# Performance work log

Hardware: AMD Instinct MI355X
Metric: run time of the kernel (lower is better)

The kernel has to match this reference:

```python
import jax, jax.numpy as jnp
import numpy as np

N_A, N_B = 50000, 10000
E = 300000
IN_F, HID, BEL_OUT, INC_OUT = 256, 256, 128, 128


def _gconv(x_src, W, b, src, dst, n_src, n_dst):
    """DGL GraphConv with norm='both': D_in^{-1/2} A D_out^{-1/2} X W + b, degs clamped to >=1."""
    ones = jnp.ones(src.shape[0], x_src.dtype)
    deg_out = jnp.maximum(jax.ops.segment_sum(ones, src, num_segments=n_src), 1.0)
    deg_in = jnp.maximum(jax.ops.segment_sum(ones, dst, num_segments=n_dst), 1.0)
    h = (x_src * jax.lax.rsqrt(deg_out)[:, None]) @ W        # [n_src, out]
    agg = jax.ops.segment_sum(h[src], dst, num_segments=n_dst)  # scatter-add messages
    return agg * jax.lax.rsqrt(deg_in)[:, None] + b


def setup_inputs() -> dict:
    key = jax.random.key(0)
    ks = jax.random.split(key, 12)
    s = 1.0 / np.sqrt(IN_F)
    sh = 1.0 / np.sqrt(HID)
    return {
        "x_a": jax.random.normal(ks[0], (N_A, IN_F), jnp.float32),
        "x_b": jax.random.normal(ks[1], (N_B, IN_F), jnp.float32),
        "W1_bel": jax.random.normal(ks[2], (IN_F, HID), jnp.float32) * s,
        "b1_bel": jnp.zeros((HID,), jnp.float32),
        "W1_inc": jax.random.normal(ks[3], (IN_F, HID), jnp.float32) * s,
        "b1_inc": jnp.zeros((HID,), jnp.float32),
        "W2_bel": jax.random.normal(ks[4], (HID, BEL_OUT), jnp.float32) * sh,
        "b2_bel": jnp.zeros((BEL_OUT,), jnp.float32),
        "W2_inc": jax.random.normal(ks[5], (HID, INC_OUT), jnp.float32) * sh,
        "b2_inc": jnp.zeros((INC_OUT,), jnp.float32),
        "bel_src": jax.random.randint(ks[6], (E,), 0, N_A, jnp.int32),
        "bel_dst": jax.random.randint(ks[7], (E,), 0, N_B, jnp.int32),
        "inc_src": jax.random.randint(ks[8], (E,), 0, N_B, jnp.int32),
        "inc_dst": jax.random.randint(ks[9], (E,), 0, N_A, jnp.int32),
    }


def reference(x_a, x_b, W1_bel, b1_bel, W1_inc, b1_inc, W2_bel, b2_bel,
              W2_inc, b2_inc, bel_src, bel_dst, inc_src, inc_dst):
    n_a, n_b = x_a.shape[0], x_b.shape[0]
    # layer 1 (HeteroGraphConv, mean over a single relation per dst type = identity)
    h_b = _gconv(x_a, W1_bel, b1_bel, bel_src, bel_dst, n_a, n_b)  # 'belongs_to': A->B
    h_a = _gconv(x_b, W1_inc, b1_inc, inc_src, inc_dst, n_b, n_a)  # 'including' : B->A
    h_a = jax.nn.relu(h_a)
    h_b = jax.nn.relu(h_b)
    # layer 2
    out_b = _gconv(h_a, W2_bel, b2_bel, bel_src, bel_dst, n_a, n_b)  # [N_B, bel_out]
    out_a = _gconv(h_b, W2_inc, b2_inc, inc_src, inc_dst, n_b, n_a)  # [N_A, inc_out]
    return out_a, out_b
```

## Files before the change

### kernel.cpp

```cpp
#include <hip/hip_runtime.h>


#define NA 50000
#define NB 10000
#define NE 300000
#define CVTB 400

typedef unsigned short u16;
typedef unsigned int u32;
typedef __attribute__((ext_vector_type(8))) short short8;
typedef __attribute__((ext_vector_type(4))) float f32x4;
typedef __attribute__((ext_vector_type(2))) float f32x2;
typedef __attribute__((ext_vector_type(4))) unsigned short u16x4;
typedef __attribute__((ext_vector_type(2))) unsigned short u16x2;

__device__ __forceinline__ float bf2f(u16 h){
  union { u32 u; float f; } x; x.u = ((u32)h) << 16; return x.f;
}
__device__ __forceinline__ u16 f2bf(float f){
  union { float f; u32 u; } x; x.f = f;
  u32 r = (x.u + 0x7FFFu + ((x.u >> 16) & 1u)) >> 16;
  return (u16)r;
}

__global__ __launch_bounds__(256) void setup0_kernel(
    int* __restrict__ z, int nz,
    const float* __restrict__ W1b, const float* __restrict__ W1i,
    const float* __restrict__ W2b, const float* __restrict__ W2i,
    u16* __restrict__ pwh, u16* __restrict__ pwl){
  int g = blockIdx.x * blockDim.x + threadIdx.x;
  int s = gridDim.x * blockDim.x;
  for (int i = g; i < nz; i += s) z[i] = 0;
  const int total = 65536 + 65536 + 32768 + 32768;
  for (int t = g; t < total; t += s){
    const float* W; int N; int tt;
    if (t < 65536)       { W = W1b; N = 256; tt = t; }
    else if (t < 131072) { W = W1i; N = 256; tt = t - 65536; }
    else if (t < 163840) { W = W2b; N = 128; tt = t - 131072; }
    else                 { W = W2i; N = 128; tt = t - 163840; }
    int j = tt & 7, lane = (tt >> 3) & 63, tile = tt >> 9;
    int nT = N >> 4;
    int nt = tile % nT, kt = tile / nT;
    int k = kt * 32 + ((lane >> 4) << 3) + j;
    int n = nt * 16 + (lane & 15);
    float v = W[k * N + n];
    u16 hi = f2bf(v);
    pwh[t] = hi;
    pwl[t] = f2bf(v - bf2f(hi));
  }
}

__global__ void hist_kernel(const int* __restrict__ bs, const int* __restrict__ bd,
                            const int* __restrict__ isc, const int* __restrict__ idt,
                            int* __restrict__ c_bs, int* __restrict__ c_bd,
                            int* __restrict__ c_is, int* __restrict__ c_id){
  int g = blockIdx.x * blockDim.x + threadIdx.x;
  int s = gridDim.x * blockDim.x;
  for (int e = g; e < NE; e += s){
    atomicAdd(&c_bs[bs[e]], 1);
    atomicAdd(&c_bd[bd[e]], 1);
    atomicAdd(&c_is[isc[e]], 1);
    atomicAdd(&c_id[idt[e]], 1);
  }
}

__global__ __launch_bounds__(1024) void scan_scales_kernel(
    const int* __restrict__ c_bs, const int* __restrict__ c_bd,
    const int* __restrict__ c_is, const int* __restrict__ c_id,
    int* __restrict__ off_bel, int* __restrict__ off_inc,
    float* __restrict__ s_ob, float* __restrict__ s_ib,
    float* __restrict__ s_oi, float* __restrict__ s_ii){
  if (blockIdx.x >= 2){
    int g = (blockIdx.x - 2) * blockDim.x + threadIdx.x;
    int s = (gridDim.x - 2) * blockDim.x;
    for (int i = g; i < NA; i += s){
      int a = c_bs[i]; s_ob[i] = rsqrtf((float)(a > 1 ? a : 1));
      int b = c_id[i]; s_ii[i] = rsqrtf((float)(b > 1 ? b : 1));
      if (i < NB){
        int c = c_bd[i]; s_ib[i] = rsqrtf((float)(c > 1 ? c : 1));
        int d = c_is[i]; s_oi[i] = rsqrtf((float)(d > 1 ? d : 1));
      }
    }
    return;
  }
  const int* cnt; int* off; int n;
  if (blockIdx.x == 0){ cnt = c_bd; off = off_bel; n = NB; }
  else                { cnt = c_id; off = off_inc; n = NA; }
  __shared__ int wsum[16];
  __shared__ int carry, chunkTot;
  int tid = threadIdx.x, lane = tid & 63, wid = tid >> 6;
  if (tid == 0) carry = 0;
  __syncthreads();
  for (int base = 0; base < n; base += 4096){
    int i0 = base + tid * 4;
    int v[4];
#pragma unroll
    for (int r = 0; r < 4; ++r){ int idx = i0 + r; v[r] = (idx < n) ? cnt[idx] : 0; }
    int s = v[0] + v[1] + v[2] + v[3];
    int x = s;
#pragma unroll
    for (int d = 1; d < 64; d <<= 1){ int t = __shfl_up(x, d, 64); if (lane >= d) x += t; }
    if (lane == 63) wsum[wid] = x;
    __syncthreads();
    if (wid == 0){
      int ws = (lane < 16) ? wsum[lane] : 0;
#pragma unroll
      for (int d = 1; d < 16; d <<= 1){ int t = __shfl_up(ws, d, 64); if (lane >= d) ws += t; }
      if (lane < 16) wsum[lane] = ws;
      if (lane == 15) chunkTot = ws;
    }
    __syncthreads();
    int waveBase = (wid == 0) ? 0 : wsum[wid - 1];
    int run = carry + waveBase + (x - s);
#pragma unroll
    for (int r = 0; r < 4; ++r){ int idx = i0 + r; if (idx < n) off[idx] = run; run += v[r]; }
    __syncthreads();
    if (tid == 0) carry += chunkTot;
    __syncthreads();
  }
  if (tid == 0) off[n] = carry;
}

__global__ __launch_bounds__(256) void cvt_fill_kernel(
    const float* __restrict__ xa, const float* __restrict__ s_ob,
    u16* __restrict__ xa16,
    const int* __restrict__ bs, const int* __restrict__ bd,
    const int* __restrict__ isc, const int* __restrict__ idt,
    const int* __restrict__ off_bel, const int* __restrict__ off_inc,
    int* __restrict__ cur_bel, int* __restrict__ cur_inc,
    int* __restrict__ csr_bel, int* __restrict__ csr_inc){
  if (blockIdx.x < CVTB){
    int g = (blockIdx.x * blockDim.x + threadIdx.x) * 4;
    int s = CVTB * blockDim.x * 4;
    for (int i = g; i < NA * 256; i += s){
      float4 v = *(const float4*)(xa + i);
      float sc = s_ob[i >> 8];
      u16x4 o;
      o.x = f2bf(v.x * sc); o.y = f2bf(v.y * sc);
      o.z = f2bf(v.z * sc); o.w = f2bf(v.w * sc);
      __builtin_nontemporal_store(o, (u16x4*)(xa16 + i));
    }
  } else {
    int g = (blockIdx.x - CVTB) * blockDim.x + threadIdx.x;
    int s = (gridDim.x - CVTB) * blockDim.x;
    for (int e = g; e < NE; e += s){
      int d0 = bd[e];
      int p0 = off_bel[d0] + atomicAdd(&cur_bel[d0], 1);
      csr_bel[p0] = bs[e];
      int d1 = idt[e];
      int p1 = off_inc[d1] + atomicAdd(&cur_inc[d1], 1);
      csr_inc[p1] = isc[e];
    }
  }
}

__global__ __launch_bounds__(256) void agg_bel_kernel(
    const u16* __restrict__ X, const int* __restrict__ off,
    const int* __restrict__ csr, float* __restrict__ Pf, int nDst){
  int wave = blockIdx.x * 4 + (threadIdx.x >> 6);
  int lane = threadIdx.x & 63;
  if (wave >= nDst) return;
  int b0 = off[wave], b1 = off[wave + 1];
  int deg = b1 - b0;
  int part = lane >> 5;
  int cl = lane & 31;
  int c = cl * 8;
  float acc[8];
#pragma unroll
  for (int q = 0; q < 8; ++q) acc[q] = 0.f;
  int idx = 0;
  if (lane < deg) idx = csr[b0 + lane];
  int lim = deg < 64 ? deg : 64;
  for (int u = 0; u < lim; u += 8){
    const u16* addr[4]; float w[4];
#pragma unroll
    for (int k = 0; k < 4; ++k){
      int e = u + k * 2 + part;
      int t = e < lim ? e : 0;
      int s0 = __shfl(idx, t, 64);
      w[k] = e < lim ? 1.f : 0.f;
      addr[k] = X + (size_t)s0 * 256 + c;
    }
    short8 v[4];
#pragma unroll
    for (int k = 0; k < 4; ++k) v[k] = *(const short8*)addr[k];
#pragma unroll
    for (int k = 0; k < 4; ++k)
#pragma unroll
      for (int q = 0; q < 8; ++q) acc[q] += bf2f((u16)v[k][q]) * w[k];
  }
  for (int j = b0 + 64 + part; j < b1; j += 2){
    int s0 = csr[j];
    short8 v0 = *(const short8*)(X + (size_t)s0 * 256 + c);
#pragma unroll
    for (int q = 0; q < 8; ++q) acc[q] += bf2f((u16)v0[q]);
  }
#pragma unroll
  for (int q = 0; q < 8; ++q) acc[q] += __shfl_xor(acc[q], 32, 64);
  if (part == 0){
    f32x4 f0 = {acc[0], acc[1], acc[2], acc[3]};
    f32x4 f1 = {acc[4], acc[5], acc[6], acc[7]};
    __builtin_nontemporal_store(f0, (f32x4*)(Pf + (size_t)wave * 256 + c));
    __builtin_nontemporal_store(f1, (f32x4*)(Pf + (size_t)wave * 256 + c + 4));
  }
}

__global__ __launch_bounds__(256) void agg_inc2_kernel(
    const u16* __restrict__ G12, const int* __restrict__ off,
    const int* __restrict__ csr,
    const float* __restrict__ s_ii, const float* __restrict__ s_ob,
    const float* __restrict__ b1i, const float* __restrict__ b2i,
    u16* __restrict__ Ha, float* __restrict__ outa){
  int wave = blockIdx.x * 4 + (threadIdx.x >> 6);
  int lane = threadIdx.x & 63;
  if (wave >= NA) return;
  int b0 = off[wave], b1 = off[wave + 1];
  int deg = b1 - b0;
  int c1 = lane * 4;
  int c2 = lane * 2;
  float acc[6];
#pragma unroll
  for (int q = 0; q < 6; ++q) acc[q] = 0.f;
  int idx = 0;
  if (lane < deg) idx = csr[b0 + lane];
  int lim = deg < 64 ? deg : 64;
  for (int u = 0; u < lim; u += 4){
    ushort4 va[4]; ushort2 vb[4]; float w[4];
#pragma unroll
    for (int k = 0; k < 4; ++k){
      int e = u + k;
      int t = e < lim ? e : 0;
      int se = __shfl(idx, t, 64);
      w[k] = e < lim ? 1.f : 0.f;
      const u16* r = G12 + (size_t)se * 384;
      va[k] = *(const ushort4*)(r + c1);
      vb[k] = *(const ushort2*)(r + 256 + c2);
    }
#pragma unroll
    for (int k = 0; k < 4; ++k){
      acc[0] += bf2f(va[k].x) * w[k];
      acc[1] += bf2f(va[k].y) * w[k];
      acc[2] += bf2f(va[k].z) * w[k];
      acc[3] += bf2f(va[k].w) * w[k];
      acc[4] += bf2f(vb[k].x) * w[k];
      acc[5] += bf2f(vb[k].y) * w[k];
    }
  }
  for (int j = b0 + 64; j < b1; ++j){
    int se = csr[j];
    const u16* r = G12 + (size_t)se * 384;
    ushort4 va = *(const ushort4*)(r + c1);
    ushort2 vb = *(const ushort2*)(r + 256 + c2);
    acc[0] += bf2f(va.x); acc[1] += bf2f(va.y);
    acc[2] += bf2f(va.z); acc[3] += bf2f(va.w);
    acc[4] += bf2f(vb.x); acc[5] += bf2f(vb.y);
  }
  float sii = s_ii[wave], sob = s_ob[wave];
  float4 bb1 = *(const float4*)(b1i + c1);
  f32x2 bb2 = *(const f32x2*)(b2i + c2);
  u16x4 o1;
  o1.x = f2bf(fmaxf(acc[0] * sii + bb1.x, 0.f) * sob);
  o1.y = f2bf(fmaxf(acc[1] * sii + bb1.y, 0.f) * sob);
  o1.z = f2bf(fmaxf(acc[2] * sii + bb1.z, 0.f) * sob);
  o1.w = f2bf(fmaxf(acc[3] * sii + bb1.w, 0.f) * sob);
  __builtin_nontemporal_store(o1, (u16x4*)(Ha + (size_t)wave * 256 + c1));
  f32x2 o2 = {acc[4] * sii + bb2.x, acc[5] * sii + bb2.y};
  __builtin_nontemporal_store(o2, (f32x2*)(outa + (size_t)wave * 128 + c2));
}

__global__ __launch_bounds__(256) void gemm_kernel(
    const float* __restrict__ A,
    const u16* __restrict__ PWH, const u16* __restrict__ PWL,
    const float* __restrict__ bias, const float* __restrict__ rs,
    float* __restrict__ Cf, u16* __restrict__ C16,
    int M, int nT, int wpsShift, int doRelu, int ldC, int colOff){
  int wave = blockIdx.x * 4 + (threadIdx.x >> 6);
  int lane = threadIdx.x & 63;
  int strips = M >> 4;
  int strip = wave >> wpsShift;
  if (strip >= strips) return;
  int slice = wave & ((1 << wpsShift) - 1);
  int ntPer = nT >> wpsShift;
  int ntStart = slice * ntPer;
  int r16 = lane & 15, quad = lane >> 4;
  int m0 = strip << 4;
  const float* aBase = A + (size_t)(m0 + r16) * 256 + quad * 8;
  short8 ah[8], al[8];
#pragma unroll
  for (int kt = 0; kt < 8; ++kt){
    float4 p0 = *(const float4*)(aBase + kt * 32);
    float4 p1 = *(const float4*)(aBase + kt * 32 + 4);
    float v[8] = {p0.x, p0.y, p0.z, p0.w, p1.x, p1.y, p1.z, p1.w};
    short8 h, l;
#pragma unroll
    for (int j = 0; j < 8; ++j){
      u16 hb = f2bf(v[j]);
      h[j] = (short)hb;
      l[j] = (short)f2bf(v[j] - bf2f(hb));
    }
    ah[kt] = h; al[kt] = l;
  }
  float rscale[4];
#pragma unroll
  for (int r = 0; r < 4; ++r) rscale[r] = rs ? rs[m0 + quad * 4 + r] : 1.f;
  for (int nt = ntStart; nt < ntStart + ntPer; ++nt){
    f32x4 acc = {0.f, 0.f, 0.f, 0.f};
    const u16* bh = PWH + ((size_t)nt * 64 + lane) * 8;
    const u16* bl = PWL + ((size_t)nt * 64 + lane) * 8;
#pragma unroll
    for (int kt = 0; kt < 8; ++kt){
      short8 wh = *(const short8*)(bh + (size_t)kt * nT * 512);
      short8 wl = *(const short8*)(bl + (size_t)kt * nT * 512);
      acc = __builtin_amdgcn_mfma_f32_16x16x32_bf16(ah[kt], wh, acc, 0, 0, 0);
      acc = __builtin_amdgcn_mfma_f32_16x16x32_bf16(al[kt], wh, acc, 0, 0, 0);
      acc = __builtin_amdgcn_mfma_f32_16x16x32_bf16(ah[kt], wl, acc, 0, 0, 0);
    }
    int col = nt * 16 + r16;
    float bv = bias ? bias[col] : 0.f;
#pragma unroll
    for (int r = 0; r < 4; ++r){
      float v = acc[r] * rscale[r] + bv;
      if (doRelu) v = fmaxf(v, 0.f);
      size_t o = (size_t)(m0 + quad * 4 + r) * ldC + colOff + col;
      if (C16) __builtin_nontemporal_store(f2bf(v), C16 + o);
      else     __builtin_nontemporal_store(v, Cf + o);
    }
  }
}

extern "C" void kernel_launch(void* const* d_in, const int* in_sizes, int n_in,
                              void* d_out, int out_size, void* d_ws, size_t ws_size,
                              hipStream_t stream){
  const float* x_a = (const float*)d_in[0];
  const float* x_b = (const float*)d_in[1];
  const float* W1b = (const float*)d_in[2];
  const float* b1b = (const float*)d_in[3];
  const float* W1i = (const float*)d_in[4];
  const float* b1i = (const float*)d_in[5];
  const float* W2b = (const float*)d_in[6];
  const float* b2b = (const float*)d_in[7];
  const float* W2i = (const float*)d_in[8];
  const float* b2i = (const float*)d_in[9];
  const int* bs  = (const int*)d_in[10];
  const int* bd  = (const int*)d_in[11];
  const int* isc = (const int*)d_in[12];
  const int* idt = (const int*)d_in[13];

  char* w = (char*)d_ws;
  size_t o = 0;
  auto take = [&](size_t bytes) -> void* {
    void* p = w + o; o = (o + bytes + 255) & ~(size_t)255; return p;
  };
  int* zint = (int*)take(180000 * sizeof(int));
  int* c_bs = zint, *c_bd = zint + 50000, *c_is = zint + 60000, *c_id = zint + 70000;
  int* cur_bel = zint + 120000, *cur_inc = zint + 130000;
  int* off_bel = (int*)take((NB + 1) * sizeof(int));
  int* off_inc = (int*)take((NA + 1) * sizeof(int));
  int* csr_bel = (int*)take(NE * sizeof(int));
  int* csr_inc = (int*)take(NE * sizeof(int));
  float* s_ob = (float*)take(NA * sizeof(float));
  float* s_ib = (float*)take(NB * sizeof(float));
  float* s_oi = (float*)take(NB * sizeof(float));
  float* s_ii = (float*)take(NA * sizeof(float));
  u16* pwh = (u16*)take(196608 * sizeof(u16));
  u16* pwl = (u16*)take(196608 * sizeof(u16));
  u16* pwh1b = pwh, *pwh1i = pwh + 65536, *pwh2b = pwh + 131072, *pwh2i = pwh + 163840;
  u16* pwl1b = pwl, *pwl1i = pwl + 65536, *pwl2b = pwl + 131072, *pwl2i = pwl + 163840;
  u16* xa16 = (u16*)take((size_t)NA * 256 * sizeof(u16));
  u16* G12  = (u16*)take((size_t)NB * 384 * sizeof(u16));
  u16* H_a  = (u16*)take((size_t)NA * 256 * sizeof(u16));
  float* P_b = (float*)take((size_t)NB * 256 * sizeof(float));
  float* H_b = (float*)take((size_t)NB * 256 * sizeof(float));

  float* out_a = (float*)d_out;
  float* out_b = (float*)d_out + (size_t)NA * 128;

  setup0_kernel<<<512, 256, 0, stream>>>(zint, 180000, W1b, W1i, W2b, W2i, pwh, pwl);
  hist_kernel<<<1172, 256, 0, stream>>>(bs, bd, isc, idt, c_bs, c_bd, c_is, c_id);
  scan_scales_kernel<<<52, 1024, 0, stream>>>(c_bs, c_bd, c_is, c_id,
                                              off_bel, off_inc,
                                              s_ob, s_ib, s_oi, s_ii);
  cvt_fill_kernel<<<CVTB + 1172, 256, 0, stream>>>(x_a, s_ob, xa16,
                                                   bs, bd, isc, idt,
                                                   off_bel, off_inc,
                                                   cur_bel, cur_inc,
                                                   csr_bel, csr_inc);

  gemm_kernel<<<625, 256, 0, stream>>>(x_b, pwh1i, pwl1i, nullptr, s_oi,
                                       nullptr, G12, NB, 16, 2, 0, 384, 0);
  agg_bel_kernel<<<2500, 256, 0, stream>>>(xa16, off_bel, csr_bel, P_b, NB);
  gemm_kernel<<<625, 256, 0, stream>>>(P_b, pwh1b, pwl1b, b1b, s_ib,
                                       H_b, nullptr, NB, 16, 2, 1, 256, 0);
  gemm_kernel<<<625, 256, 0, stream>>>(H_b, pwh2i, pwl2i, nullptr, s_oi,
                                       nullptr, G12, NB, 8, 2, 0, 384, 256);
  agg_inc2_kernel<<<12500, 256, 0, stream>>>(G12, off_inc, csr_inc,
                                             s_ii, s_ob, b1i, b2i, H_a, out_a);
  agg_bel_kernel<<<2500, 256, 0, stream>>>(H_a, off_bel, csr_bel, P_b, NB);
  gemm_kernel<<<625, 256, 0, stream>>>(P_b, pwh2b, pwl2b, b2b, s_ib,
                                       out_b, nullptr, NB, 8, 2, 0, 128, 0);
}
```

Measured before the change: 432.0 us.

## Record atomic ranks in histogram, overlap x_a conversion, apply out-degree scale in aggregation

The histogram kernel now stores each edge's atomic rank within its destination bucket, so CSR fill becomes an atomic-free scatter using offset plus rank. The x_a to bf16 conversion moves into the histogram launch, because it no longer needs the out-degree scale and can run alongside the histogram. The scale is instead applied per source edge inside the first bel aggregation, which adds a gather of s_ob per edge. The change also adds two rank arrays the size of the edge list, costing extra memory traffic.

Result: faster. 409.4 us (-5.2%).

```diff
diff --git a/kernel.cpp b/kernel.cpp
--- a/kernel.cpp
+++ b/kernel.cpp
@@ -4,6 +4,7 @@
 #define NA 50000
 #define NB 10000
 #define NE 300000
+#define HB 1172
 #define CVTB 400
 
 typedef unsigned short u16;
@@ -12,7 +13,6 @@
 typedef __attribute__((ext_vector_type(4))) float f32x4;
 typedef __attribute__((ext_vector_type(2))) float f32x2;
 typedef __attribute__((ext_vector_type(4))) unsigned short u16x4;
-typedef __attribute__((ext_vector_type(2))) unsigned short u16x2;
 
 __device__ __forceinline__ float bf2f(u16 h){
   union { u32 u; float f; } x; x.u = ((u32)h) << 16; return x.f;
@@ -50,17 +50,31 @@
   }
 }
 
-__global__ void hist_kernel(const int* __restrict__ bs, const int* __restrict__ bd,
-                            const int* __restrict__ isc, const int* __restrict__ idt,
-                            int* __restrict__ c_bs, int* __restrict__ c_bd,
-                            int* __restrict__ c_is, int* __restrict__ c_id){
-  int g = blockIdx.x * blockDim.x + threadIdx.x;
-  int s = gridDim.x * blockDim.x;
-  for (int e = g; e < NE; e += s){
-    atomicAdd(&c_bs[bs[e]], 1);
-    atomicAdd(&c_bd[bd[e]], 1);
-    atomicAdd(&c_is[isc[e]], 1);
-    atomicAdd(&c_id[idt[e]], 1);
+__global__ __launch_bounds__(256) void histcvt_kernel(
+    const int* __restrict__ bs, const int* __restrict__ bd,
+    const int* __restrict__ isc, const int* __restrict__ idt,
+    int* __restrict__ c_bs, int* __restrict__ c_bd,
+    int* __restrict__ c_is, int* __restrict__ c_id,
+    int* __restrict__ rank_bel, int* __restrict__ rank_inc,
+    const float* __restrict__ xa, u16* __restrict__ xa16){
+  if (blockIdx.x < HB){
+    int g = blockIdx.x * blockDim.x + threadIdx.x;
+    int s = HB * blockDim.x;
+    for (int e = g; e < NE; e += s){
+      atomicAdd(&c_bs[bs[e]], 1);
+      rank_bel[e] = atomicAdd(&c_bd[bd[e]], 1);
+      atomicAdd(&c_is[isc[e]], 1);
+      rank_inc[e] = atomicAdd(&c_id[idt[e]], 1);
+    }
+  } else {
+    int g = ((blockIdx.x - HB) * blockDim.x + threadIdx.x) * 4;
+    int s = CVTB * blockDim.x * 4;
+    for (int i = g; i < NA * 256; i += s){
+      float4 v = *(const float4*)(xa + i);
+      u16x4 o;
+      o.x = f2bf(v.x); o.y = f2bf(v.y); o.z = f2bf(v.z); o.w = f2bf(v.w);
+      __builtin_nontemporal_store(o, (u16x4*)(xa16 + i));
+    }
   }
 }
 
@@ -121,42 +135,24 @@
   if (tid == 0) off[n] = carry;
 }
 
-__global__ __launch_bounds__(256) void cvt_fill_kernel(
-    const float* __restrict__ xa, const float* __restrict__ s_ob,
-    u16* __restrict__ xa16,
+__global__ __launch_bounds__(256) void fill_kernel(
     const int* __restrict__ bs, const int* __restrict__ bd,
     const int* __restrict__ isc, const int* __restrict__ idt,
+    const int* __restrict__ rank_bel, const int* __restrict__ rank_inc,
     const int* __restrict__ off_bel, const int* __restrict__ off_inc,
-    int* __restrict__ cur_bel, int* __restrict__ cur_inc,
     int* __restrict__ csr_bel, int* __restrict__ csr_inc){
-  if (blockIdx.x < CVTB){
-    int g = (blockIdx.x * blockDim.x + threadIdx.x) * 4;
-    int s = CVTB * blockDim.x * 4;
-    for (int i = g; i < NA * 256; i += s){
-      float4 v = *(const float4*)(xa + i);
-      float sc = s_ob[i >> 8];
-      u16x4 o;
-      o.x = f2bf(v.x * sc); o.y = f2bf(v.y * sc);
-      o.z = f2bf(v.z * sc); o.w = f2bf(v.w * sc);
-      __builtin_nontemporal_store(o, (u16x4*)(xa16 + i));
-    }
-  } else {
-    int g = (blockIdx.x - CVTB) * blockDim.x + threadIdx.x;
-    int s = (gridDim.x - CVTB) * blockDim.x;
-    for (int e = g; e < NE; e += s){
-      int d0 = bd[e];
-      int p0 = off_bel[d0] + atomicAdd(&cur_bel[d0], 1);
-      csr_bel[p0] = bs[e];
-      int d1 = idt[e];
-      int p1 = off_inc[d1] + atomicAdd(&cur_inc[d1], 1);
-      csr_inc[p1] = isc[e];
-    }
+  int g = blockIdx.x * blockDim.x + threadIdx.x;
+  int s = gridDim.x * blockDim.x;
+  for (int e = g; e < NE; e += s){
+    csr_bel[off_bel[bd[e]] + rank_bel[e]] = bs[e];
+    csr_inc[off_inc[idt[e]] + rank_inc[e]] = isc[e];
   }
 }
 
 __global__ __launch_bounds__(256) void agg_bel_kernel(
-    const u16* __restrict__ X, const int* __restrict__ off,
-    const int* __restrict__ csr, float* __restrict__ Pf, int nDst){
+    const u16* __restrict__ X, const float* __restrict__ ss,
+    const int* __restrict__ off, const int* __restrict__ csr,
+    float* __restrict__ Pf, int nDst){
   int wave = blockIdx.x * 4 + (threadIdx.x >> 6);
   int lane = threadIdx.x & 63;
   if (wave >= nDst) return;
@@ -168,8 +164,11 @@
   float acc[8];
 #pragma unroll
   for (int q = 0; q < 8; ++q) acc[q] = 0.f;
-  int idx = 0;
-  if (lane < deg) idx = csr[b0 + lane];
+  int idx = 0; float sc = 0.f;
+  if (lane < deg){
+    idx = csr[b0 + lane];
+    sc = ss ? ss[idx] : 1.f;
+  }
   int lim = deg < 64 ? deg : 64;
   for (int u = 0; u < lim; u += 8){
     const u16* addr[4]; float w[4];
@@ -178,7 +177,8 @@
       int e = u + k * 2 + part;
       int t = e < lim ? e : 0;
       int s0 = __shfl(idx, t, 64);
-      w[k] = e < lim ? 1.f : 0.f;
+      float c0 = __shfl(sc, t, 64);
+      w[k] = e < lim ? c0 : 0.f;
       addr[k] = X + (size_t)s0 * 256 + c;
     }
     short8 v[4];
@@ -191,9 +191,10 @@
   }
   for (int j = b0 + 64 + part; j < b1; j += 2){
     int s0 = csr[j];
+    float c0 = ss ? ss[s0] : 1.f;
     short8 v0 = *(const short8*)(X + (size_t)s0 * 256 + c);
 #pragma unroll
-    for (int q = 0; q < 8; ++q) acc[q] += bf2f((u16)v0[q]);
+    for (int q = 0; q < 8; ++q) acc[q] += bf2f((u16)v0[q]) * c0;
   }
 #pragma unroll
   for (int q = 0; q < 8; ++q) acc[q] += __shfl_xor(acc[q], 32, 64);
@@ -351,9 +352,10 @@
   auto take = [&](size_t bytes) -> void* {
     void* p = w + o; o = (o + bytes + 255) & ~(size_t)255; return p;
   };
-  int* zint = (int*)take(180000 * sizeof(int));
+  int* zint = (int*)take(120000 * sizeof(int));
   int* c_bs = zint, *c_bd = zint + 50000, *c_is = zint + 60000, *c_id = zint + 70000;
-  int* cur_bel = zint + 120000, *cur_inc = zint + 130000;
+  int* rank_bel = (int*)take(NE * sizeof(int));
+  int* rank_inc = (int*)take(NE * sizeof(int));
   int* off_bel = (int*)take((NB + 1) * sizeof(int));
   int* off_inc = (int*)take((NA + 1) * sizeof(int));
   int* csr_bel = (int*)take(NE * sizeof(int));
@@ -375,27 +377,26 @@
   float* out_a = (float*)d_out;
   float* out_b = (float*)d_out + (size_t)NA * 128;
 
-  setup0_kernel<<<512, 256, 0, stream>>>(zint, 180000, W1b, W1i, W2b, W2i, pwh, pwl);
-  hist_kernel<<<1172, 256, 0, stream>>>(bs, bd, isc, idt, c_bs, c_bd, c_is, c_id);
+  setup0_kernel<<<512, 256, 0, stream>>>(zint, 120000, W1b, W1i, W2b, W2i, pwh, pwl);
+  histcvt_kernel<<<HB + CVTB, 256, 0, stream>>>(bs, bd, isc, idt,
+                                                c_bs, c_bd, c_is, c_id,
+                                                rank_bel, rank_inc, x_a, xa16);
   scan_scales_kernel<<<52, 1024, 0, stream>>>(c_bs, c_bd, c_is, c_id,
                                               off_bel, off_inc,
                                               s_ob, s_ib, s_oi, s_ii);
-  cvt_fill_kernel<<<CVTB + 1172, 256, 0, stream>>>(x_a, s_ob, xa16,
-                                                   bs, bd, isc, idt,
-                                                   off_bel, off_inc,
-                                                   cur_bel, cur_inc,
-                                                   csr_bel, csr_inc);
+  fill_kernel<<<1172, 256, 0, stream>>>(bs, bd, isc, idt, rank_bel, rank_inc,
+                                        off_bel, off_inc, csr_bel, csr_inc);
 
   gemm_kernel<<<625, 256, 0, stream>>>(x_b, pwh1i, pwl1i, nullptr, s_oi,
                                        nullptr, G12, NB, 16, 2, 0, 384, 0);
-  agg_bel_kernel<<<2500, 256, 0, stream>>>(xa16, off_bel, csr_bel, P_b, NB);
+  agg_bel_kernel<<<2500, 256, 0, stream>>>(xa16, s_ob, off_bel, csr_bel, P_b, NB);
   gemm_kernel<<<625, 256, 0, stream>>>(P_b, pwh1b, pwl1b, b1b, s_ib,
                                        H_b, nullptr, NB, 16, 2, 1, 256, 0);
   gemm_kernel<<<625, 256, 0, stream>>>(H_b, pwh2i, pwl2i, nullptr, s_oi,
                                        nullptr, G12, NB, 8, 2, 0, 384, 256);
   agg_inc2_kernel<<<12500, 256, 0, stream>>>(G12, off_inc, csr_inc,
                                              s_ii, s_ob, b1i, b2i, H_a, out_a);
-  agg_bel_kernel<<<2500, 256, 0, stream>>>(H_a, off_bel, csr_bel, P_b, NB);
+  agg_bel_kernel<<<2500, 256, 0, stream>>>(H_a, nullptr, off_bel, csr_bel, P_b, NB);
   gemm_kernel<<<625, 256, 0, stream>>>(P_b, pwh2b, pwl2b, b2b, s_ib,
                                        out_b, nullptr, NB, 8, 2, 0, 128, 0);
 }
```
